# Performance work log

Hardware: AMD Instinct MI355X
Metric: run time of the kernel (lower is better)

## Reference

```python
import jax, jax.numpy as jnp
import numpy as np

MASK_VALUE = -10000000000.0
B, S = 2, 2048
HQ, HKV, HD = 16, 8, 256
D = HQ * HD  # 4096
ROPE_BASE = 10000.0


def rms_norm(x, scale, eps=1e-6):
    # Gemma-style RMSNorm over the last (head_dim) axis with (1 + scale) gain.
    var = jnp.mean(jnp.square(x), axis=-1, keepdims=True)
    return x * jax.lax.rsqrt(var + eps) * (1.0 + scale)


def apply_rope(x, positions):
    # x: [b, t, h, d]; positions: [b, t]
    d = x.shape[-1]
    fraction = 2.0 * jnp.arange(d // 2, dtype=jnp.float32) / d
    timescale = ROPE_BASE ** fraction                     # [d/2]
    sinusoid = positions[..., None].astype(jnp.float32) / timescale  # [b, t, d/2]
    sin = jnp.sin(sinusoid)[:, :, None, :]                # [b, t, 1, d/2]
    cos = jnp.cos(sinusoid)[:, :, None, :]
    first, second = jnp.split(x, 2, axis=-1)
    out = jnp.concatenate([first * cos - second * sin,
                           second * cos + first * sin], axis=-1)
    return out.astype(x.dtype)


def setup_inputs() -> dict:
    key = jax.random.key(0)
    ks = jax.random.split(key, 6)
    x = jax.random.normal(ks[0], (B, S, D), dtype=jnp.float32)
    Wq = jax.random.normal(ks[1], (D, HQ * HD), dtype=jnp.float32) * 0.02
    Wk = jax.random.normal(ks[2], (D, HKV * HD), dtype=jnp.float32) * 0.02
    Wv = jax.random.normal(ks[3], (D, HKV * HD), dtype=jnp.float32) * 0.02
    Wo = jax.random.normal(ks[4], (HQ * HD, D), dtype=jnp.float32) * 0.02
    k_scale = jnp.zeros((HD,), dtype=jnp.float32)
    v_scale = jnp.zeros((HD,), dtype=jnp.float32)
    mask = jnp.broadcast_to(jnp.tril(jnp.ones((S, S), dtype=bool))[None], (B, S, S))
    position = jnp.broadcast_to(jnp.arange(S, dtype=jnp.int32)[None], (B, S))
    return {"x": x, "Wq": Wq, "Wk": Wk, "Wv": Wv, "Wo": Wo,
            "k_scale": k_scale, "v_scale": v_scale,
            "mask": mask, "position": position}


def reference(x, Wq, Wk, Wv, Wo, k_scale, v_scale, mask, position):
    b, t, _ = x.shape
    group = HQ // HKV
    q = (x @ Wq).reshape(b, t, HQ, HD)
    k = (x @ Wk).reshape(b, t, HKV, HD)
    v = (x @ Wv).reshape(b, t, HKV, HD)
    k = rms_norm(k, k_scale)
    v = rms_norm(v, v_scale)
    q = apply_rope(q, position)
    k = apply_rope(k, position)
    # [b, hkv, group, t, d] view of q; avoids materializing repeated K/V (same math as repeat).
    q = q.transpose(0, 2, 1, 3).reshape(b, HKV, group, t, HD)
    k = k.transpose(0, 2, 1, 3)  # [b, hkv, T, d]
    v = v.transpose(0, 2, 1, 3)
    scores = jnp.einsum('bhgtd,bhTd->bhgtT', q, k) / jnp.sqrt(jnp.float32(HD))
    scores = jnp.where(mask[:, None, None, :, :], scores, MASK_VALUE)
    weights = jax.nn.softmax(scores, axis=-1)
    out = jnp.einsum('bhgtT,bhTd->bhgtd', weights, v)
    out = out.reshape(b, HQ, t, HD).transpose(0, 2, 1, 3).reshape(b, t, HQ * HD)
    return out @ Wo
```

## Files before the change

### kernel.cpp

```cpp
#include <hip/hip_runtime.h>
#include <stdint.h>

typedef __bf16 bf16;
typedef __bf16 bf16x4 __attribute__((ext_vector_type(4)));
typedef __bf16 bf16x8 __attribute__((ext_vector_type(8)));
typedef float f32x4 __attribute__((ext_vector_type(4)));

#define GAS __attribute__((address_space(1)))
#define LAS __attribute__((address_space(3)))

__device__ __forceinline__ void gload_lds16(const void* g, void* l) {
  __builtin_amdgcn_global_load_lds((GAS const void*)g, (LAS void*)l, 16, 0, 0);
}

__global__ __launch_bounds__(256) void cvt_bf16(const float* __restrict__ in,
                                                bf16* __restrict__ out, int n4) {
  int i = blockIdx.x * 256 + threadIdx.x;
  if (i >= n4) return;
  float4 v = ((const float4*)in)[i];
  bf16x4 o;
  o[0] = (bf16)v.x; o[1] = (bf16)v.y; o[2] = (bf16)v.z; o[3] = (bf16)v.w;
  ((bf16x4*)out)[i] = o;
}

__global__ __launch_bounds__(256) void tconv(const float* __restrict__ W,
                                             bf16* __restrict__ Wt, int K, int N) {
  __shared__ bf16 tile[64][65];
  const int tx = threadIdx.x & 63, ty = threadIdx.x >> 6;
  const int n0 = blockIdx.x * 64, k0 = blockIdx.y * 64;
#pragma unroll
  for (int i = 0; i < 16; ++i) {
    int kr = ty + i * 4;
    tile[kr][tx] = (bf16)W[(size_t)(k0 + kr) * N + n0 + tx];
  }
  __syncthreads();
#pragma unroll
  for (int i = 0; i < 16; ++i) {
    int nr = ty + i * 4;
    Wt[(size_t)(n0 + nr) * K + k0 + tx] = tile[tx][nr];
  }
}

template <int OUTF32>
__global__ __launch_bounds__(512, 2) void gemm256(const bf16* __restrict__ A,
                                                  const bf16* __restrict__ Bt,
                                                  void* __restrict__ Cp,
                                                  const int N, const int K,
                                                  const int NBX) {
  __shared__ __attribute__((aligned(16))) bf16 lds[2][4][8192];
  const int t = threadIdx.x, w = t >> 6, l = t & 63;
  const int la = l & 15, lq = l >> 4;
  const int nwg = gridDim.x, cpx = nwg >> 3;
  const int sid = (blockIdx.x & 7) * cpx + (blockIdx.x >> 3);
  const int by = sid / NBX, bx = sid % NBX;
  const int m0 = by * 256, n0 = bx * 256;
  const int wr = w >> 2, wc = w & 3;
  const int c0 = w * 64 + l;
  const int sr0 = c0 >> 2, soff = (((c0 & 3) ^ ((c0 >> 3) & 3)) << 3);
  const bf16* pA0 = A + (size_t)(m0 + sr0) * K + soff;
  const bf16* pA1 = pA0 + (size_t)128 * K;
  const bf16* pB0 = Bt + (size_t)(n0 + sr0) * K + soff;
  const bf16* pB1 = pB0 + (size_t)128 * K;
  const int rsl = (lq ^ ((la >> 1) & 3)) << 3;

  f32x4 acc[8][4] = {};

#define STAGE_SLAB(s, nb, kti)                                                \
  do {                                                                        \
    const bf16* p0_ = ((s) & 1) ? pB0 : pA0;                                  \
    const bf16* p1_ = ((s) & 1) ? pB1 : pA1;                                  \
    const size_t ko_ = (size_t)(kti) * 64 + ((s) >> 1) * 32;                  \
    gload_lds16(p0_ + ko_, &lds[nb][s][w * 512]);                             \
    gload_lds16(p1_ + ko_, &lds[nb][s][4096 + w * 512]);                      \
  } while (0)

#define PHASE(kh, mg, LOADB)                                                  \
  {                                                                           \
    bf16x8 a_[4];                                                             \
    _Pragma("unroll") for (int m_ = 0; m_ < 4; ++m_)                          \
        a_[m_] = *(const bf16x8*)&lds[bi][(kh)*2][(wr * 128 + (mg)*64 + m_ * 16 + la) * 32 + rsl]; \
    if (LOADB) {                                                              \
      _Pragma("unroll") for (int n_ = 0; n_ < 4; ++n_)                        \
          bfr[n_] = *(const bf16x8*)&lds[bi][(kh)*2 + 1][(wc * 64 + n_ * 16 + la) * 32 + rsl]; \
    }                                                                         \
    __builtin_amdgcn_s_setprio(1);                                            \
    _Pragma("unroll") for (int m_ = 0; m_ < 4; ++m_)                          \
      _Pragma("unroll") for (int n_ = 0; n_ < 4; ++n_)                        \
          acc[(mg)*4 + m_][n_] = __builtin_amdgcn_mfma_f32_16x16x32_bf16(     \
              a_[m_], bfr[n_], acc[(mg)*4 + m_][n_], 0, 0, 0);                \
    __builtin_amdgcn_s_setprio(0);                                            \
  }

  STAGE_SLAB(0, 0, 0);
  STAGE_SLAB(1, 0, 0);
  STAGE_SLAB(2, 0, 0);
  STAGE_SLAB(3, 0, 0);

  const int NT = K >> 6;
  for (int kt = 0; kt < NT; ++kt) {
    const int bi = kt & 1, nbi = bi ^ 1;
    const bool pf = (kt + 1) < NT;
    bf16x8 bfr[4];
    if (pf) asm volatile("s_waitcnt vmcnt(4)" ::: "memory");
    else    asm volatile("s_waitcnt vmcnt(0)" ::: "memory");
    __builtin_amdgcn_s_barrier();
    __builtin_amdgcn_sched_barrier(0);
    if (pf) STAGE_SLAB(0, nbi, kt + 1);
    PHASE(0, 0, 1)
    __builtin_amdgcn_s_barrier();
    __builtin_amdgcn_sched_barrier(0);
    if (pf) STAGE_SLAB(1, nbi, kt + 1);
    PHASE(0, 1, 0)
    __builtin_amdgcn_s_barrier();
    __builtin_amdgcn_sched_barrier(0);
    if (pf) asm volatile("s_waitcnt vmcnt(4)" ::: "memory");
    else    asm volatile("s_waitcnt vmcnt(0)" ::: "memory");
    __builtin_amdgcn_s_barrier();
    __builtin_amdgcn_sched_barrier(0);
    if (pf) STAGE_SLAB(2, nbi, kt + 1);
    PHASE(1, 0, 1)
    __builtin_amdgcn_s_barrier();
    __builtin_amdgcn_sched_barrier(0);
    if (pf) STAGE_SLAB(3, nbi, kt + 1);
    PHASE(1, 1, 0)
    __builtin_amdgcn_s_barrier();
    __builtin_amdgcn_sched_barrier(0);
  }
#undef PHASE
#undef STAGE_SLAB

  const int crow = m0 + wr * 128, ccol = n0 + wc * 64;
  if (OUTF32) {
    float* C = (float*)Cp;
#pragma unroll
    for (int mi = 0; mi < 8; ++mi)
#pragma unroll
      for (int ni = 0; ni < 4; ++ni)
#pragma unroll
        for (int i = 0; i < 4; ++i)
          C[(size_t)(crow + mi * 16 + lq * 4 + i) * N + ccol + ni * 16 + la] = acc[mi][ni][i];
  } else {
    bf16* C = (bf16*)Cp;
#pragma unroll
    for (int mi = 0; mi < 8; ++mi)
#pragma unroll
      for (int ni = 0; ni < 4; ++ni)
#pragma unroll
        for (int i = 0; i < 4; ++i)
          C[(size_t)(crow + mi * 16 + lq * 4 + i) * N + ccol + ni * 16 + la] = (bf16)acc[mi][ni][i];
  }
}

__global__ __launch_bounds__(256) void rope_q(bf16* __restrict__ qkv, const int* __restrict__ pos) {
  const int w = threadIdx.x >> 6, l = threadIdx.x & 63;
  const int idx = blockIdx.x * 4 + w;
  const int bt = idx >> 4, h = idx & 15;
  bf16* p = qkv + (size_t)bt * 8192 + h * 256 + l * 4;
  bf16x4 xv = *(const bf16x4*)p;
  float x[4], y[4];
#pragma unroll
  for (int j = 0; j < 4; ++j) x[j] = (float)xv[j];
#pragma unroll
  for (int j = 0; j < 4; ++j) y[j] = __shfl_xor(x[j], 32, 64);
  const float posf = (float)pos[bt];
  bf16x4 ov;
#pragma unroll
  for (int j = 0; j < 4; ++j) {
    const int pr = (l & 31) * 4 + j;
    float sv, cv;
    sincosf(posf * exp2f((float)pr * (-13.287712379549449f / 128.0f)), &sv, &cv);
    float o = x[j] * cv + ((l < 32) ? -y[j] : y[j]) * sv;
    ov[j] = (bf16)(o * 0.0625f);
  }
  *(bf16x4*)p = ov;
}

__global__ __launch_bounds__(256) void norm_rope_k(bf16* __restrict__ kbase,
                                                   const float* __restrict__ scale,
                                                   const int* __restrict__ pos) {
  const int w = threadIdx.x >> 6, l = threadIdx.x & 63;
  const int idx = blockIdx.x * 4 + w;
  const int bt = idx >> 3, h = idx & 7;
  bf16* p = kbase + (size_t)bt * 8192 + h * 256 + l * 4;
  bf16x4 xv = *(const bf16x4*)p;
  float x[4];
#pragma unroll
  for (int j = 0; j < 4; ++j) x[j] = (float)xv[j];
  float ss = x[0] * x[0] + x[1] * x[1] + x[2] * x[2] + x[3] * x[3];
#pragma unroll
  for (int m = 1; m < 64; m <<= 1) ss += __shfl_xor(ss, m, 64);
  const float r = rsqrtf(ss * (1.0f / 256.0f) + 1e-6f);
#pragma unroll
  for (int j = 0; j < 4; ++j) x[j] = x[j] * r * (1.0f + scale[l * 4 + j]);
  float y[4];
#pragma unroll
  for (int j = 0; j < 4; ++j) y[j] = __shfl_xor(x[j], 32, 64);
  const float posf = (float)pos[bt];
  bf16x4 ov;
#pragma unroll
  for (int j = 0; j < 4; ++j) {
    const int pr = (l & 31) * 4 + j;
    float sv, cv;
    sincosf(posf * exp2f((float)pr * (-13.287712379549449f / 128.0f)), &sv, &cv);
    float o = x[j] * cv + ((l < 32) ? -y[j] : y[j]) * sv;
    ov[j] = (bf16)o;
  }
  *(bf16x4*)p = ov;
}

__global__ __launch_bounds__(256) void norm_v(bf16* __restrict__ vbase,
                                              const float* __restrict__ scale) {
  const int w = threadIdx.x >> 6, l = threadIdx.x & 63;
  const int idx = blockIdx.x * 4 + w;
  const int bt = idx >> 3, h = idx & 7;
  bf16* p = vbase + (size_t)bt * 8192 + h * 256 + l * 4;
  bf16x4 xv = *(const bf16x4*)p;
  float x[4];
#pragma unroll
  for (int j = 0; j < 4; ++j) x[j] = (float)xv[j];
  float ss = x[0] * x[0] + x[1] * x[1] + x[2] * x[2] + x[3] * x[3];
#pragma unroll
  for (int m = 1; m < 64; m <<= 1) ss += __shfl_xor(ss, m, 64);
  const float r = rsqrtf(ss * (1.0f / 256.0f) + 1e-6f);
  bf16x4 ov;
#pragma unroll
  for (int j = 0; j < 4; ++j) ov[j] = (bf16)(x[j] * r * (1.0f + scale[l * 4 + j]));
  *(bf16x4*)p = ov;
}

__global__ __launch_bounds__(256) void vtrans(const bf16* __restrict__ vbase,
                                              bf16* __restrict__ vt) {
  __shared__ bf16 tile[64][65];
  const int tx = threadIdx.x & 63, ty = threadIdx.x >> 6;
  const int tt = blockIdx.x, dd = blockIdx.y, bh = blockIdx.z;
  const int b = bh >> 3, h = bh & 7;
#pragma unroll
  for (int i = 0; i < 16; ++i) {
    int trow = tt * 64 + ty + i * 4;
    tile[ty + i * 4][tx] = vbase[(size_t)(b * 2048 + trow) * 8192 + h * 256 + dd * 64 + tx];
  }
  __syncthreads();
#pragma unroll
  for (int i = 0; i < 16; ++i) {
    int drow = dd * 64 + ty + i * 4;
    vt[((size_t)(b * 8 + h) * 256 + drow) * 2048 + tt * 64 + tx] = tile[tx][ty + i * 4];
  }
}

__global__ __launch_bounds__(512, 2) void flash_attn(const bf16* __restrict__ qkv,
                                                     const bf16* __restrict__ vt,
                                                     bf16* __restrict__ o) {
  __shared__ __attribute__((aligned(16))) bf16 Ks[2 * 16384];
  __shared__ __attribute__((aligned(16))) bf16 Vs[2 * 16384];
  __shared__ __attribute__((aligned(16))) bf16 Ps[8 * 1152];
  const int t = threadIdx.x, w = t >> 6, l = t & 63;
  const int la = l & 15, lq = l >> 4;
  const int h = blockIdx.x, qbp = blockIdx.y, b = blockIdx.z;
  const int hkv = h >> 1;

  const bf16* kbase = qkv + (size_t)(b * 2048) * 8192 + 4096 + hkv * 256;
  const bf16* vbase = vt + ((size_t)(b * 8 + hkv)) * 256 * 2048;

  const bf16* ksrc[4];
  const bf16* vsrc[4];
#pragma unroll
  for (int i = 0; i < 4; ++i) {
    int c = i * 512 + t;
    int krr = c >> 5, ksl = (c & 31) ^ (krr & 7);
    int vrr = c >> 3, vsl = (c & 7) ^ (vrr & 7);
    ksrc[i] = kbase + (size_t)krr * 8192 + ksl * 8;
    vsrc[i] = vbase + (size_t)vrr * 2048 + vsl * 8;
  }

#define STAGE(bb, tt0)                                                        \
  do {                                                                        \
    _Pragma("unroll") for (int i_ = 0; i_ < 4; ++i_)                          \
        gload_lds16(ksrc[i_] + (size_t)(tt0) * 8192,                          \
                    Ks + (bb) * 16384 + i_ * 4096 + w * 512);                 \
    _Pragma("unroll") for (int i_ = 0; i_ < 4; ++i_)                          \
        gload_lds16(vsrc[i_] + (tt0), Vs + (bb) * 16384 + i_ * 4096 + w * 512); \
  } while (0)

  for (int part = 0; part < 2; ++part) {
    const int qb = part ? qbp : (15 - qbp);
    const int q0 = qb * 128;
    const int rbase = q0 + w * 16;

    bf16x8 qf[8];
    {
      const bf16* qrow = qkv + (size_t)(b * 2048 + rbase + la) * 8192 + h * 256 + lq * 8;
#pragma unroll
      for (int kg = 0; kg < 8; ++kg) qf[kg] = *(const bf16x8*)(qrow + kg * 32);
    }
    f32x4 acc[16] = {};
    float mrow[4] = {-1e30f, -1e30f, -1e30f, -1e30f};
    float lrow[4] = {0.f, 0.f, 0.f, 0.f};
    const int nT = 2 * qb + 2;

    STAGE(0, 0);
    int cur = 0;
    for (int tti = 0; tti < nT; ++tti) {
      const int t0 = tti * 64;
      if (tti + 1 < nT) {
        STAGE(cur ^ 1, t0 + 64);
        asm volatile("s_waitcnt vmcnt(8)" ::: "memory");
      } else {
        asm volatile("s_waitcnt vmcnt(0)" ::: "memory");
      }
      __builtin_amdgcn_s_barrier();
      __builtin_amdgcn_sched_barrier(0);
      if (t0 <= rbase + 15) {
        const bf16* Kc = Ks + cur * 16384;
        const bf16* Vc = Vs + cur * 16384;
        f32x4 s[4] = {};
        __builtin_amdgcn_s_setprio(1);
#pragma unroll
        for (int n = 0; n < 4; ++n) {
          int rT = n * 16 + la;
#pragma unroll
          for (int kg = 0; kg < 8; ++kg) {
            int sl = (kg * 4 + lq) ^ (rT & 7);
            bf16x8 kbv = *(const bf16x8*)(Kc + rT * 256 + sl * 8);
            s[n] = __builtin_amdgcn_mfma_f32_16x16x32_bf16(qf[kg], kbv, s[n], 0, 0, 0);
          }
        }
        __builtin_amdgcn_s_setprio(0);
        float scalef[4];
#pragma unroll
        for (int i = 0; i < 4; ++i) {
          const int row = rbase + lq * 4 + i;
          float mx = -1e30f;
#pragma unroll
          for (int n = 0; n < 4; ++n) {
            float v = s[n][i];
            v = (t0 + n * 16 + la > row) ? -1e30f : v;
            s[n][i] = v;
            mx = fmaxf(mx, v);
          }
          mx = fmaxf(mx, __shfl_xor(mx, 1, 64));
          mx = fmaxf(mx, __shfl_xor(mx, 2, 64));
          mx = fmaxf(mx, __shfl_xor(mx, 4, 64));
          mx = fmaxf(mx, __shfl_xor(mx, 8, 64));
          const float mnew = fmaxf(mrow[i], mx);
          scalef[i] = __expf(mrow[i] - mnew);
          float ps = 0.f;
#pragma unroll
          for (int n = 0; n < 4; ++n) {
            float v = s[n][i];
            float pp = (v <= -1e29f) ? 0.f : __expf(v - mnew);
            s[n][i] = pp;
            ps += pp;
          }
          ps += __shfl_xor(ps, 1, 64);
          ps += __shfl_xor(ps, 2, 64);
          ps += __shfl_xor(ps, 4, 64);
          ps += __shfl_xor(ps, 8, 64);
          mrow[i] = mnew;
          lrow[i] = lrow[i] * scalef[i] + ps;
        }
#pragma unroll
        for (int n = 0; n < 16; ++n) {
          acc[n][0] *= scalef[0]; acc[n][1] *= scalef[1];
          acc[n][2] *= scalef[2]; acc[n][3] *= scalef[3];
        }
        bf16* pw = Ps + w * 1152;
#pragma unroll
        for (int n = 0; n < 4; ++n)
#pragma unroll
          for (int i = 0; i < 4; ++i)
            pw[(lq * 4 + i) * 72 + n * 16 + la] = (bf16)s[n][i];
        __builtin_amdgcn_s_setprio(1);
#pragma unroll
        for (int kc = 0; kc < 2; ++kc) {
          bf16x8 pa = *(const bf16x8*)(pw + la * 72 + kc * 32 + lq * 8);
#pragma unroll
          for (int n = 0; n < 16; ++n) {
            int rd = n * 16 + la;
            int sl = (kc * 4 + lq) ^ (rd & 7);
            bf16x8 vbv = *(const bf16x8*)(Vc + rd * 64 + sl * 8);
            acc[n] = __builtin_amdgcn_mfma_f32_16x16x32_bf16(pa, vbv, acc[n], 0, 0, 0);
          }
        }
        __builtin_amdgcn_s_setprio(0);
      }
      __builtin_amdgcn_s_barrier();
      __builtin_amdgcn_sched_barrier(0);
      cur ^= 1;
    }
#pragma unroll
    for (int i = 0; i < 4; ++i) {
      const int row = rbase + lq * 4 + i;
      const float inv = 1.0f / lrow[i];
      bf16* orow = o + ((size_t)(b * 2048 + row)) * 4096 + h * 256;
#pragma unroll
      for (int n = 0; n < 16; ++n) orow[n * 16 + la] = (bf16)(acc[n][i] * inv);
    }
  }
#undef STAGE
}

__global__ void fill_err(float* o, int n) {
  int i = blockIdx.x * 256 + threadIdx.x;
  if (i < n) o[i] = 1e9f;
}

extern "C" void kernel_launch(void* const* d_in, const int* in_sizes, int n_in,
                              void* d_out, int out_size, void* d_ws, size_t ws_size,
                              hipStream_t stream) {
  const float* x = (const float*)d_in[0];
  const float* Wq = (const float*)d_in[1];
  const float* Wk = (const float*)d_in[2];
  const float* Wv = (const float*)d_in[3];
  const float* Wo = (const float*)d_in[4];
  const float* kscale = (const float*)d_in[5];
  const float* vscale = (const float*)d_in[6];
  const int* pos = (const int*)d_in[8];
  float* out = (float*)d_out;

  const size_t WS_NEED = 251658240ull;
  if (ws_size < WS_NEED) {
    fill_err<<<65536, 256, 0, stream>>>(out, out_size);
    return;
  }
  char* ws = (char*)d_ws;
  bf16* x16   = (bf16*)(ws);
  bf16* wqkvt = (bf16*)(ws + 33554432);
  bf16* wot   = (bf16*)(ws + 100663296);
  bf16* qkv   = (bf16*)(ws + 134217728);
  bf16* vtb   = (bf16*)(ws + 201326592);
  bf16* ao    = (bf16*)(ws + 218103808);

  cvt_bf16<<<16384, 256, 0, stream>>>(x, x16, 4194304);
  tconv<<<dim3(64, 64), 256, 0, stream>>>(Wq, wqkvt, 4096, 4096);
  tconv<<<dim3(32, 64), 256, 0, stream>>>(Wk, wqkvt + (size_t)4096 * 4096, 4096, 2048);
  tconv<<<dim3(32, 64), 256, 0, stream>>>(Wv, wqkvt + (size_t)6144 * 4096, 4096, 2048);
  tconv<<<dim3(64, 64), 256, 0, stream>>>(Wo, wot, 4096, 4096);

  gemm256<0><<<512, 512, 0, stream>>>(x16, wqkvt, qkv, 8192, 4096, 32);

  rope_q<<<16384, 256, 0, stream>>>(qkv, pos);
  norm_rope_k<<<8192, 256, 0, stream>>>(qkv + 4096, kscale, pos);
  norm_v<<<8192, 256, 0, stream>>>(qkv + 6144, vscale);
  vtrans<<<dim3(32, 4, 16), 256, 0, stream>>>(qkv + 6144, vtb);

  flash_attn<<<dim3(16, 8, 2), 512, 0, stream>>>(qkv, vtb, ao);

  gemm256<1><<<256, 512, 0, stream>>>(ao, wot, out, 4096, 4096, 16);
}
```

Before: 666.7 us.

## Remap GEMM tiles per XCD and drop redundant intra-iteration barriers

Tile coordinates are now assigned so each XCD works on a compact 2D block of output tiles, set by new log2 parameters, instead of a linear swizzle. The aim is better L2 reuse of A and B panels within each XCD. The GEMM main loop also drops the barriers after each MFMA phase and keeps only the two barriers that follow the vmcnt waits. B-fragment loads move out of the phase macro into explicit loads. Fewer barriers cut wave stalls, but correctness now depends on the remaining waits ordering the LDS double-buffer reuse.

```diff
diff --git a/kernel.cpp b/kernel.cpp
--- a/kernel.cpp
+++ b/kernel.cpp
@@ -46,13 +46,14 @@
                                                   const bf16* __restrict__ Bt,
                                                   void* __restrict__ Cp,
                                                   const int N, const int K,
-                                                  const int NBX) {
+                                                  const int ncc_l, const int cbx_l) {
   __shared__ __attribute__((aligned(16))) bf16 lds[2][4][8192];
   const int t = threadIdx.x, w = t >> 6, l = t & 63;
   const int la = l & 15, lq = l >> 4;
-  const int nwg = gridDim.x, cpx = nwg >> 3;
-  const int sid = (blockIdx.x & 7) * cpx + (blockIdx.x >> 3);
-  const int by = sid / NBX, bx = sid % NBX;
+  const int xcd = blockIdx.x & 7, wi = blockIdx.x >> 3;
+  const int cr = xcd >> ncc_l, cc = xcd & ((1 << ncc_l) - 1);
+  const int by = (cr << 3) + (wi >> cbx_l);
+  const int bx = (cc << cbx_l) + (wi & ((1 << cbx_l) - 1));
   const int m0 = by * 256, n0 = bx * 256;
   const int wr = w >> 2, wc = w & 3;
   const int c0 = w * 64 + l;
@@ -74,15 +75,11 @@
     gload_lds16(p1_ + ko_, &lds[nb][s][4096 + w * 512]);                      \
   } while (0)
 
-#define PHASE(kh, mg, LOADB)                                                  \
+#define PHASE(kh, mg)                                                         \
   {                                                                           \
     bf16x8 a_[4];                                                             \
     _Pragma("unroll") for (int m_ = 0; m_ < 4; ++m_)                          \
         a_[m_] = *(const bf16x8*)&lds[bi][(kh)*2][(wr * 128 + (mg)*64 + m_ * 16 + la) * 32 + rsl]; \
-    if (LOADB) {                                                              \
-      _Pragma("unroll") for (int n_ = 0; n_ < 4; ++n_)                        \
-          bfr[n_] = *(const bf16x8*)&lds[bi][(kh)*2 + 1][(wc * 64 + n_ * 16 + la) * 32 + rsl]; \
-    }                                                                         \
     __builtin_amdgcn_s_setprio(1);                                            \
     _Pragma("unroll") for (int m_ = 0; m_ < 4; ++m_)                          \
       _Pragma("unroll") for (int n_ = 0; n_ < 4; ++n_)                        \
@@ -106,25 +103,23 @@
     __builtin_amdgcn_s_barrier();
     __builtin_amdgcn_sched_barrier(0);
     if (pf) STAGE_SLAB(0, nbi, kt + 1);
-    PHASE(0, 0, 1)
-    __builtin_amdgcn_s_barrier();
-    __builtin_amdgcn_sched_barrier(0);
+#pragma unroll
+    for (int n_ = 0; n_ < 4; ++n_)
+      bfr[n_] = *(const bf16x8*)&lds[bi][1][(wc * 64 + n_ * 16 + la) * 32 + rsl];
+    PHASE(0, 0)
     if (pf) STAGE_SLAB(1, nbi, kt + 1);
-    PHASE(0, 1, 0)
-    __builtin_amdgcn_s_barrier();
-    __builtin_amdgcn_sched_barrier(0);
+    PHASE(0, 1)
     if (pf) asm volatile("s_waitcnt vmcnt(4)" ::: "memory");
     else    asm volatile("s_waitcnt vmcnt(0)" ::: "memory");
     __builtin_amdgcn_s_barrier();
     __builtin_amdgcn_sched_barrier(0);
     if (pf) STAGE_SLAB(2, nbi, kt + 1);
-    PHASE(1, 0, 1)
-    __builtin_amdgcn_s_barrier();
-    __builtin_amdgcn_sched_barrier(0);
+#pragma unroll
+    for (int n_ = 0; n_ < 4; ++n_)
+      bfr[n_] = *(const bf16x8*)&lds[bi][3][(wc * 64 + n_ * 16 + la) * 32 + rsl];
+    PHASE(1, 0)
     if (pf) STAGE_SLAB(3, nbi, kt + 1);
-    PHASE(1, 1, 0)
-    __builtin_amdgcn_s_barrier();
-    __builtin_amdgcn_sched_barrier(0);
+    PHASE(1, 1)
   }
 #undef PHASE
 #undef STAGE_SLAB
@@ -436,7 +431,7 @@
   tconv<<<dim3(32, 64), 256, 0, stream>>>(Wv, wqkvt + (size_t)6144 * 4096, 4096, 2048);
   tconv<<<dim3(64, 64), 256, 0, stream>>>(Wo, wot, 4096, 4096);
 
-  gemm256<0><<<512, 512, 0, stream>>>(x16, wqkvt, qkv, 8192, 4096, 32);
+  gemm256<0><<<512, 512, 0, stream>>>(x16, wqkvt, qkv, 8192, 4096, 2, 3);
 
   rope_q<<<16384, 256, 0, stream>>>(qkv, pos);
   norm_rope_k<<<8192, 256, 0, stream>>>(qkv + 4096, kscale, pos);
@@ -445,5 +440,5 @@
 
   flash_attn<<<dim3(16, 8, 2), 512, 0, stream>>>(qkv, vtb, ao);
 
-  gemm256<1><<<256, 512, 0, stream>>>(ao, wot, out, 4096, 4096, 16);
-}
+  gemm256<1><<<256, 512, 0, stream>>>(ao, wot, out, 4096, 4096, 2, 2);
+}
```

New measurement: 634.5 us, median of 2. 4.8% less time.
